# Kernel optimization log

Measured on AMD Instinct MI355X. Metric: run time of the kernel, lower is better.

Reference implementation:

```python
import jax, jax.numpy as jnp
import numpy as np

N = 100000
K = 10  # number of propagation hops


def setup_inputs() -> dict:
    key = jax.random.key(0)
    k1, k2, k3, k4 = jax.random.split(key, 4)
    E, D = 3200000, 128
    feats = jax.random.normal(k1, (N, D), dtype=jnp.float32)
    s = jax.random.normal(k2, (D, 1), dtype=jnp.float32) * 0.1
    src = jax.random.randint(k3, (E,), 0, N, dtype=jnp.int32)
    dst = jax.random.randint(k4, (E,), 0, N, dtype=jnp.int32)
    return {"feats": feats, "s": s, "src": src, "dst": dst}


def reference(feats, s, src, dst):
    # degrees (in-degree = count of dst, out-degree = count of src)
    ones = jnp.ones(src.shape[0], dtype=jnp.float32)
    in_deg = jax.ops.segment_sum(ones, dst, num_segments=N)
    out_deg = jax.ops.segment_sum(ones, src, num_segments=N)
    dst_norm = jnp.clip(in_deg, 1.0, None) ** -0.5  # [N]
    src_norm = jnp.clip(out_deg, 1.0, None) ** -0.5  # [N]
    dst_norm = dst_norm[:, None]
    src_norm = src_norm[:, None]

    results = [feats]
    h = feats
    for _ in range(K):
        h = h * src_norm                                  # [N, D]
        msg = h[src]                                      # gather  [E, D]
        h = jax.ops.segment_sum(msg, dst, num_segments=N)  # scatter [N, D]
        h = h * dst_norm
        results.append(h)

    H = jnp.stack(results, axis=1)                 # [N, K+1, D]
    S = jax.nn.sigmoid(jnp.matmul(H, s))           # [N, K+1, 1]
    S = jnp.transpose(S, (0, 2, 1))                # [N, 1, K+1]
    out = jnp.matmul(S, H).squeeze()               # [N, D]
    return out
```

## Files before the change

### kernel.cpp

```cpp
#include <hip/hip_runtime.h>
#include <hip/hip_fp16.h>

#define NODES 100000
#define DIM 128
#define KSTEPS 10
#define CAP 128

#define RSHIFT 11
#define RANGE 2048
#define NR 49
#define GBCAP 72000
#define VPT 16
#define BT (256 * VPT)

__global__ void bucket_agg(const int* __restrict__ src, const int* __restrict__ dst,
                           unsigned* __restrict__ gdc, unsigned* __restrict__ gsc,
                           unsigned* __restrict__ dpairs, unsigned* __restrict__ spairs, int E) {
    __shared__ unsigned dcnt[NR], scnt[NR], dbase[NR], sbase[NR];
    const int tid = threadIdx.x;
    if (tid < NR) { dcnt[tid] = 0; scnt[tid] = 0; }
    __syncthreads();

    const int base = blockIdx.x * BT;
    int dv[VPT], sv[VPT];
    unsigned rd[VPT], rs[VPT];
    #pragma unroll
    for (int j = 0; j < VPT; ++j) {
        int i = base + tid + j * 256;
        if (i < E) {
            int d_ = dst[i]; int s_ = src[i];
            dv[j] = d_; sv[j] = s_;
            rd[j] = atomicAdd(&dcnt[d_ >> RSHIFT], 1u);
            rs[j] = atomicAdd(&scnt[s_ >> RSHIFT], 1u);
        }
    }
    __syncthreads();
    if (tid < NR) {
        unsigned c = dcnt[tid];
        dbase[tid] = c ? atomicAdd(&gdc[tid], c) : 0u;
    } else if (tid >= 64 && tid < 64 + NR) {
        int b = tid - 64;
        unsigned c = scnt[b];
        sbase[b] = c ? atomicAdd(&gsc[b], c) : 0u;
    }
    __syncthreads();
    #pragma unroll
    for (int j = 0; j < VPT; ++j) {
        int i = base + tid + j * 256;
        if (i < E) {
            int d_ = dv[j]; int s_ = sv[j];
            int b = d_ >> RSHIFT;
            unsigned pos = dbase[b] + rd[j];
            if (pos < GBCAP)
                dpairs[(size_t)b * GBCAP + pos] =
                    ((unsigned)s_ << RSHIFT) | (unsigned)(d_ & (RANGE - 1));
            int bs = s_ >> RSHIFT;
            unsigned ps = sbase[bs] + rs[j];
            if (ps < GBCAP)
                spairs[(size_t)bs * GBCAP + ps] = (unsigned)(s_ & (RANGE - 1));
        }
    }
}

__global__ void degree_scatter(const unsigned* __restrict__ gdc, const unsigned* __restrict__ gsc,
                               const unsigned* __restrict__ dpairs, const unsigned* __restrict__ spairs,
                               int* __restrict__ cur, int* __restrict__ outc,
                               int* __restrict__ csr) {
    __shared__ int ctr[RANGE];
    const int r = blockIdx.x >> 1;
    const int nodebase = r << RSHIFT;
    for (int i = threadIdx.x; i < RANGE; i += blockDim.x) ctr[i] = 0;
    __syncthreads();
    if ((blockIdx.x & 1) == 0) {
        int cnt = (int)gdc[r]; if (cnt > GBCAP) cnt = GBCAP;
        const unsigned* p = dpairs + (size_t)r * GBCAP;
        for (int i = threadIdx.x; i < cnt; i += blockDim.x) {
            unsigned v = p[i];
            int dloc = (int)(v & (RANGE - 1));
            int s_ = (int)(v >> RSHIFT);
            int slot = atomicAdd(&ctr[dloc], 1);
            if (slot < CAP) csr[((size_t)(nodebase + dloc) << 7) + slot] = s_;
        }
        __syncthreads();
        for (int i = threadIdx.x; i < RANGE; i += blockDim.x) {
            int node = nodebase + i;
            if (node < NODES) cur[node] = ctr[i];
        }
    } else {
        int cnt = (int)gsc[r]; if (cnt > GBCAP) cnt = GBCAP;
        const unsigned* p = spairs + (size_t)r * GBCAP;
        for (int i = threadIdx.x; i < cnt; i += blockDim.x)
            atomicAdd(&ctr[p[i]], 1);
        __syncthreads();
        for (int i = threadIdx.x; i < RANGE; i += blockDim.x) {
            int node = nodebase + i;
            if (node < NODES) outc[node] = ctr[i];
        }
    }
}

__global__ void norm_kernel(const int* __restrict__ outc, const int* __restrict__ inc,
                            float* __restrict__ src_norm, float* __restrict__ isrc,
                            float* __restrict__ dst_norm, int n) {
    int i = blockIdx.x * blockDim.x + threadIdx.x;
    if (i < n) {
        float od = fmaxf((float)outc[i], 1.0f);
        float id = fmaxf((float)inc[i], 1.0f);
        float sn = rsqrtf(od);
        src_norm[i] = sn;
        isrc[i] = sqrtf(od);
        dst_norm[i] = rsqrtf(id);
    }
}

__global__ void combine0_main(const float* __restrict__ feats, const float* __restrict__ s,
                              const float* __restrict__ src_norm,
                              __half* __restrict__ p0, float* __restrict__ sg0, int n) {
    int lane = threadIdx.x & 63;
    int wave = (blockIdx.x * blockDim.x + threadIdx.x) >> 6;
    int nwaves = (gridDim.x * blockDim.x) >> 6;
    float2 sv = *(const float2*)(s + lane * 2);
    for (int node = wave; node < n; node += nwaves) {
        float2 hv = *(const float2*)(feats + (size_t)node * DIM + lane * 2);
        float sn = src_norm[node];
        __half2 ph; ph.x = __float2half(sn * hv.x); ph.y = __float2half(sn * hv.y);
        *(__half2*)(p0 + (size_t)node * DIM + lane * 2) = ph;
        float dot = hv.x * sv.x + hv.y * sv.y;
        #pragma unroll
        for (int off = 32; off > 0; off >>= 1) dot += __shfl_xor(dot, off);
        if (lane == 0) sg0[node] = 1.0f / (1.0f + expf(-dot));
    }
}

__global__ void combine0_fb(const float* __restrict__ feats, const float* __restrict__ s,
                            const float* __restrict__ src_norm,
                            __half* __restrict__ p0, float* __restrict__ out, int n) {
    int lane = threadIdx.x & 63;
    int wave = (blockIdx.x * blockDim.x + threadIdx.x) >> 6;
    int nwaves = (gridDim.x * blockDim.x) >> 6;
    float2 sv = *(const float2*)(s + lane * 2);
    for (int node = wave; node < n; node += nwaves) {
        float2 hv = *(const float2*)(feats + (size_t)node * DIM + lane * 2);
        float sn = src_norm[node];
        __half2 ph; ph.x = __float2half(sn * hv.x); ph.y = __float2half(sn * hv.y);
        *(__half2*)(p0 + (size_t)node * DIM + lane * 2) = ph;
        float dot = hv.x * sv.x + hv.y * sv.y;
        #pragma unroll
        for (int off = 32; off > 0; off >>= 1) dot += __shfl_xor(dot, off);
        float sg = 1.0f / (1.0f + expf(-dot));
        float2 ov; ov.x = sg * hv.x; ov.y = sg * hv.y;
        *(float2*)(out + (size_t)node * DIM + lane * 2) = ov;
    }
}

__global__ void gather_main(const __half* __restrict__ pprev,
                            const float* __restrict__ src_norm, const float* __restrict__ dst_norm,
                            const int* __restrict__ cnt, const int* __restrict__ csr,
                            const float* __restrict__ s,
                            __half* __restrict__ pnext, float* __restrict__ sgk, int n) {
    int lane = threadIdx.x & 63;
    int wave = (blockIdx.x * blockDim.x + threadIdx.x) >> 6;
    int nwaves = (gridDim.x * blockDim.x) >> 6;
    float2 sv = *(const float2*)(s + lane * 2);
    for (int node = wave; node < n; node += nwaves) {
        int c = cnt[node]; if (c > CAP) c = CAP;
        const int* row = csr + ((size_t)node << 7);
        float accx = 0.0f, accy = 0.0f;
        int p = 0;
        for (; p + 7 < c; p += 8) {
            int s0 = row[p], s1 = row[p+1], s2 = row[p+2], s3 = row[p+3];
            int s4 = row[p+4], s5 = row[p+5], s6 = row[p+6], s7 = row[p+7];
            float2 f0 = __half22float2(*(const __half2*)(pprev + (size_t)s0 * DIM + lane * 2));
            float2 f1 = __half22float2(*(const __half2*)(pprev + (size_t)s1 * DIM + lane * 2));
            float2 f2 = __half22float2(*(const __half2*)(pprev + (size_t)s2 * DIM + lane * 2));
            float2 f3 = __half22float2(*(const __half2*)(pprev + (size_t)s3 * DIM + lane * 2));
            float2 f4 = __half22float2(*(const __half2*)(pprev + (size_t)s4 * DIM + lane * 2));
            float2 f5 = __half22float2(*(const __half2*)(pprev + (size_t)s5 * DIM + lane * 2));
            float2 f6 = __half22float2(*(const __half2*)(pprev + (size_t)s6 * DIM + lane * 2));
            float2 f7 = __half22float2(*(const __half2*)(pprev + (size_t)s7 * DIM + lane * 2));
            accx += f0.x + f1.x + f2.x + f3.x + f4.x + f5.x + f6.x + f7.x;
            accy += f0.y + f1.y + f2.y + f3.y + f4.y + f5.y + f6.y + f7.y;
        }
        for (; p < c; ++p) {
            int si = row[p];
            float2 fv = __half22float2(*(const __half2*)(pprev + (size_t)si * DIM + lane * 2));
            accx += fv.x; accy += fv.y;
        }
        float dn = dst_norm[node];
        float hx = dn * accx, hy = dn * accy;
        float dot = hx * sv.x + hy * sv.y;
        #pragma unroll
        for (int off = 32; off > 0; off >>= 1) dot += __shfl_xor(dot, off);
        if (lane == 0) sgk[node] = 1.0f / (1.0f + expf(-dot));
        float sn = src_norm[node];
        __half2 pw; pw.x = __float2half(sn * hx); pw.y = __float2half(sn * hy);
        *(__half2*)(pnext + (size_t)node * DIM + lane * 2) = pw;
    }
}

__global__ void gather_fb(const __half* __restrict__ pprev,
                          const float* __restrict__ src_norm, const float* __restrict__ dst_norm,
                          const int* __restrict__ cnt, const int* __restrict__ csr,
                          const float* __restrict__ s,
                          __half* __restrict__ pnext, float* __restrict__ out, int n) {
    int lane = threadIdx.x & 63;
    int wave = (blockIdx.x * blockDim.x + threadIdx.x) >> 6;
    int nwaves = (gridDim.x * blockDim.x) >> 6;
    float2 sv = *(const float2*)(s + lane * 2);
    for (int node = wave; node < n; node += nwaves) {
        int c = cnt[node]; if (c > CAP) c = CAP;
        const int* row = csr + ((size_t)node << 7);
        float accx = 0.0f, accy = 0.0f;
        int p = 0;
        for (; p + 7 < c; p += 8) {
            int s0 = row[p], s1 = row[p+1], s2 = row[p+2], s3 = row[p+3];
            int s4 = row[p+4], s5 = row[p+5], s6 = row[p+6], s7 = row[p+7];
            float2 f0 = __half22float2(*(const __half2*)(pprev + (size_t)s0 * DIM + lane * 2));
            float2 f1 = __half22float2(*(const __half2*)(pprev + (size_t)s1 * DIM + lane * 2));
            float2 f2 = __half22float2(*(const __half2*)(pprev + (size_t)s2 * DIM + lane * 2));
            float2 f3 = __half22float2(*(const __half2*)(pprev + (size_t)s3 * DIM + lane * 2));
            float2 f4 = __half22float2(*(const __half2*)(pprev + (size_t)s4 * DIM + lane * 2));
            float2 f5 = __half22float2(*(const __half2*)(pprev + (size_t)s5 * DIM + lane * 2));
            float2 f6 = __half22float2(*(const __half2*)(pprev + (size_t)s6 * DIM + lane * 2));
            float2 f7 = __half22float2(*(const __half2*)(pprev + (size_t)s7 * DIM + lane * 2));
            accx += f0.x + f1.x + f2.x + f3.x + f4.x + f5.x + f6.x + f7.x;
            accy += f0.y + f1.y + f2.y + f3.y + f4.y + f5.y + f6.y + f7.y;
        }
        for (; p < c; ++p) {
            int si = row[p];
            float2 fv = __half22float2(*(const __half2*)(pprev + (size_t)si * DIM + lane * 2));
            accx += fv.x; accy += fv.y;
        }
        float dn = dst_norm[node];
        float hx = dn * accx, hy = dn * accy;
        float dot = hx * sv.x + hy * sv.y;
        #pragma unroll
        for (int off = 32; off > 0; off >>= 1) dot += __shfl_xor(dot, off);
        float sg = 1.0f / (1.0f + expf(-dot));
        float2 ov = *(float2*)(out + (size_t)node * DIM + lane * 2);
        ov.x += sg * hx; ov.y += sg * hy;
        *(float2*)(out + (size_t)node * DIM + lane * 2) = ov;
        float sn = src_norm[node];
        __half2 pw; pw.x = __float2half(sn * hx); pw.y = __float2half(sn * hy);
        *(__half2*)(pnext + (size_t)node * DIM + lane * 2) = pw;
    }
}

__global__ void out_accum(const __half* __restrict__ pbase, const float* __restrict__ sg,
                          const float* __restrict__ isrc, float* __restrict__ out,
                          int kstart, int count, int m, int first, int n) {
    int lane = threadIdx.x & 63;
    int wave = (blockIdx.x * blockDim.x + threadIdx.x) >> 6;
    int nwaves = (gridDim.x * blockDim.x) >> 6;
    for (int node = wave; node < n; node += nwaves) {
        float iv = isrc[node];
        float ax, ay;
        if (first) { ax = 0.0f; ay = 0.0f; }
        else {
            float2 ov = *(float2*)(out + (size_t)node * DIM + lane * 2);
            ax = ov.x; ay = ov.y;
        }
        for (int j = 0; j < count; ++j) {
            int kk = kstart + j;
            int slot = kk % m;
            float g = sg[(size_t)kk * n + node] * iv;
            float2 fv = __half22float2(
                *(const __half2*)(pbase + ((size_t)slot * n + node) * DIM + lane * 2));
            ax += g * fv.x; ay += g * fv.y;
        }
        *(float2*)(out + (size_t)node * DIM + lane * 2) = make_float2(ax, ay);
    }
}

extern "C" void kernel_launch(void* const* d_in, const int* in_sizes, int n_in,
                              void* d_out, int out_size, void* d_ws, size_t ws_size,
                              hipStream_t stream) {
    const float* feats = (const float*)d_in[0];
    const float* s     = (const float*)d_in[1];
    const int*   src   = (const int*)d_in[2];
    const int*   dst   = (const int*)d_in[3];
    float* out = (float*)d_out;
    const int E = in_sizes[2];

    int*   outc     = (int*)d_ws;
    int*   cur      = outc + NODES;
    float* src_norm = (float*)(cur + NODES);
    float* isrc     = src_norm + NODES;
    float* dst_norm = isrc + NODES;
    float* sg       = dst_norm + NODES;
    int*   csr      = (int*)(sg + (size_t)(KSTEPS + 1) * NODES);
    __half* pbase   = (__half*)(csr + (size_t)NODES * CAP);

    const size_t head_bytes = (size_t)(2 * NODES) * 4 + (size_t)(3 + KSTEPS + 1) * NODES * 4
                            + (size_t)NODES * CAP * 4;
    const size_t pbuf = (size_t)NODES * DIM * sizeof(__half);

    int m = 0;
    if (ws_size > head_bytes) m = (int)((ws_size - head_bytes) / pbuf);
    if (m > KSTEPS + 1) m = KSTEPS + 1;

    unsigned* gdc    = (unsigned*)pbase;
    unsigned* gsc    = gdc + 64;
    unsigned* dpairs = gsc + 64;
    unsigned* spairs = dpairs + (size_t)NR * GBCAP;

    hipMemsetAsync(gdc, 0, 2 * 64 * sizeof(unsigned), stream);
    const int nbatch = (E + BT - 1) / BT;
    bucket_agg<<<nbatch, 256, 0, stream>>>(src, dst, gdc, gsc, dpairs, spairs, E);
    degree_scatter<<<2 * NR, 256, 0, stream>>>(gdc, gsc, dpairs, spairs, cur, outc, csr);
    norm_kernel<<<(NODES + 255) / 256, 256, 0, stream>>>(outc, cur, src_norm, isrc, dst_norm, NODES);

    const int ngrid = (NODES * 64 + 255) / 256;
    if (m >= 2) {
        combine0_main<<<ngrid, 256, 0, stream>>>(feats, s, src_norm, pbase, sg, NODES);
        int flushed = 0;
        int first = 1;
        for (int k = 1; k <= KSTEPS; ++k) {
            if (k - flushed >= m) {
                out_accum<<<ngrid, 256, 0, stream>>>(pbase, sg, isrc, out,
                                                     flushed, k - flushed, m, first, NODES);
                flushed = k; first = 0;
            }
            const __half* pprev = pbase + (size_t)((k - 1) % m) * NODES * DIM;
            __half* pnext = pbase + (size_t)(k % m) * NODES * DIM;
            gather_main<<<ngrid, 256, 0, stream>>>(pprev, src_norm, dst_norm, cur, csr, s,
                                                   pnext, sg + (size_t)k * NODES, NODES);
        }
        out_accum<<<ngrid, 256, 0, stream>>>(pbase, sg, isrc, out,
                                             flushed, KSTEPS + 1 - flushed, m, first, NODES);
    } else {
        __half* pA = pbase;
        __half* pB = pbase + (size_t)NODES * DIM;
        combine0_fb<<<ngrid, 256, 0, stream>>>(feats, s, src_norm, pA, out, NODES);
        const __half* pcur = pA;
        for (int k = 1; k <= KSTEPS; ++k) {
            __half* pnext = (k & 1) ? pB : pA;
            gather_fb<<<ngrid, 256, 0, stream>>>(pcur, src_norm, dst_norm, cur, csr, s,
                                                 pnext, out, NODES);
            pcur = pnext;
        }
    }
}
```

Before: 1.532 ms.

## Gather four neighbor rows per wave with 16-byte loads and padded CSR

Each wave in gather_main is split into four 16-lane groups. Every group fetches a different neighbor row with uint4 loads, so each load instruction covers four edges, and the partial sums are combined afterwards with cross-group shuffles. Neighbor lists are padded to a multiple of 8 with a dummy index pointing at an extra zeroed row per feature slab, which removes the scalar tail loop. CAP drops from 128 to 96 to shrink the CSR footprint. The cost is a few extra memsets and padded loads, plus silent truncation if any node's in-degree exceeds 96.

```diff
diff --git a/kernel.cpp b/kernel.cpp
--- a/kernel.cpp
+++ b/kernel.cpp
@@ -4,7 +4,7 @@
 #define NODES 100000
 #define DIM 128
 #define KSTEPS 10
-#define CAP 128
+#define CAP 96
 
 #define RSHIFT 11
 #define RANGE 2048
@@ -12,6 +12,8 @@
 #define GBCAP 72000
 #define VPT 16
 #define BT (256 * VPT)
+
+#define SLAB ((size_t)(NODES + 1) * DIM)
 
 __global__ void bucket_agg(const int* __restrict__ src, const int* __restrict__ dst,
                            unsigned* __restrict__ gdc, unsigned* __restrict__ gsc,
@@ -79,12 +81,18 @@
             int dloc = (int)(v & (RANGE - 1));
             int s_ = (int)(v >> RSHIFT);
             int slot = atomicAdd(&ctr[dloc], 1);
-            if (slot < CAP) csr[((size_t)(nodebase + dloc) << 7) + slot] = s_;
+            if (slot < CAP) csr[(size_t)(nodebase + dloc) * CAP + slot] = s_;
         }
         __syncthreads();
         for (int i = threadIdx.x; i < RANGE; i += blockDim.x) {
             int node = nodebase + i;
-            if (node < NODES) cur[node] = ctr[i];
+            if (node < NODES) {
+                int c = ctr[i]; if (c > CAP) c = CAP;
+                cur[node] = ctr[i];
+                int cpad = (c + 7) & ~7; if (cpad > CAP) cpad = CAP;
+                for (int q = c; q < cpad; ++q)
+                    csr[(size_t)node * CAP + q] = NODES;
+            }
         }
     } else {
         int cnt = (int)gsc[r]; if (cnt > GBCAP) cnt = GBCAP;
@@ -159,42 +167,84 @@
                             const float* __restrict__ s,
                             __half* __restrict__ pnext, float* __restrict__ sgk, int n) {
     int lane = threadIdx.x & 63;
-    int wave = (blockIdx.x * blockDim.x + threadIdx.x) >> 6;
-    int nwaves = (gridDim.x * blockDim.x) >> 6;
-    float2 sv = *(const float2*)(s + lane * 2);
+    int g = lane >> 4, t = lane & 15;
+    int wave = (blockIdx.x * blockDim.x + threadIdx.x) >> 6;
+    int nwaves = (gridDim.x * blockDim.x) >> 6;
+    float4 sva = *(const float4*)(s + t * 8);
+    float4 svb = *(const float4*)(s + t * 8 + 4);
     for (int node = wave; node < n; node += nwaves) {
         int c = cnt[node]; if (c > CAP) c = CAP;
-        const int* row = csr + ((size_t)node << 7);
-        float accx = 0.0f, accy = 0.0f;
+        int cpad = (c + 7) & ~7;
+        const int* row = csr + (size_t)node * CAP;
+        float a0=0,a1=0,a2=0,a3=0,a4=0,a5=0,a6=0,a7=0;
         int p = 0;
-        for (; p + 7 < c; p += 8) {
-            int s0 = row[p], s1 = row[p+1], s2 = row[p+2], s3 = row[p+3];
-            int s4 = row[p+4], s5 = row[p+5], s6 = row[p+6], s7 = row[p+7];
-            float2 f0 = __half22float2(*(const __half2*)(pprev + (size_t)s0 * DIM + lane * 2));
-            float2 f1 = __half22float2(*(const __half2*)(pprev + (size_t)s1 * DIM + lane * 2));
-            float2 f2 = __half22float2(*(const __half2*)(pprev + (size_t)s2 * DIM + lane * 2));
-            float2 f3 = __half22float2(*(const __half2*)(pprev + (size_t)s3 * DIM + lane * 2));
-            float2 f4 = __half22float2(*(const __half2*)(pprev + (size_t)s4 * DIM + lane * 2));
-            float2 f5 = __half22float2(*(const __half2*)(pprev + (size_t)s5 * DIM + lane * 2));
-            float2 f6 = __half22float2(*(const __half2*)(pprev + (size_t)s6 * DIM + lane * 2));
-            float2 f7 = __half22float2(*(const __half2*)(pprev + (size_t)s7 * DIM + lane * 2));
-            accx += f0.x + f1.x + f2.x + f3.x + f4.x + f5.x + f6.x + f7.x;
-            accy += f0.y + f1.y + f2.y + f3.y + f4.y + f5.y + f6.y + f7.y;
-        }
-        for (; p < c; ++p) {
-            int si = row[p];
-            float2 fv = __half22float2(*(const __half2*)(pprev + (size_t)si * DIM + lane * 2));
-            accx += fv.x; accy += fv.y;
-        }
+        for (; p + 15 < cpad; p += 16) {
+            int e0 = row[p + g];
+            int e1 = row[p + 4 + g];
+            int e2 = row[p + 8 + g];
+            int e3 = row[p + 12 + g];
+            uint4 q0 = *(const uint4*)(pprev + (size_t)e0 * DIM + t * 8);
+            uint4 q1 = *(const uint4*)(pprev + (size_t)e1 * DIM + t * 8);
+            uint4 q2 = *(const uint4*)(pprev + (size_t)e2 * DIM + t * 8);
+            uint4 q3 = *(const uint4*)(pprev + (size_t)e3 * DIM + t * 8);
+            float2 f;
+            f = __half22float2(*(__half2*)&q0.x); a0+=f.x; a1+=f.y;
+            f = __half22float2(*(__half2*)&q0.y); a2+=f.x; a3+=f.y;
+            f = __half22float2(*(__half2*)&q0.z); a4+=f.x; a5+=f.y;
+            f = __half22float2(*(__half2*)&q0.w); a6+=f.x; a7+=f.y;
+            f = __half22float2(*(__half2*)&q1.x); a0+=f.x; a1+=f.y;
+            f = __half22float2(*(__half2*)&q1.y); a2+=f.x; a3+=f.y;
+            f = __half22float2(*(__half2*)&q1.z); a4+=f.x; a5+=f.y;
+            f = __half22float2(*(__half2*)&q1.w); a6+=f.x; a7+=f.y;
+            f = __half22float2(*(__half2*)&q2.x); a0+=f.x; a1+=f.y;
+            f = __half22float2(*(__half2*)&q2.y); a2+=f.x; a3+=f.y;
+            f = __half22float2(*(__half2*)&q2.z); a4+=f.x; a5+=f.y;
+            f = __half22float2(*(__half2*)&q2.w); a6+=f.x; a7+=f.y;
+            f = __half22float2(*(__half2*)&q3.x); a0+=f.x; a1+=f.y;
+            f = __half22float2(*(__half2*)&q3.y); a2+=f.x; a3+=f.y;
+            f = __half22float2(*(__half2*)&q3.z); a4+=f.x; a5+=f.y;
+            f = __half22float2(*(__half2*)&q3.w); a6+=f.x; a7+=f.y;
+        }
+        for (; p < cpad; p += 8) {
+            int e0 = row[p + g];
+            int e1 = row[p + 4 + g];
+            uint4 q0 = *(const uint4*)(pprev + (size_t)e0 * DIM + t * 8);
+            uint4 q1 = *(const uint4*)(pprev + (size_t)e1 * DIM + t * 8);
+            float2 f;
+            f = __half22float2(*(__half2*)&q0.x); a0+=f.x; a1+=f.y;
+            f = __half22float2(*(__half2*)&q0.y); a2+=f.x; a3+=f.y;
+            f = __half22float2(*(__half2*)&q0.z); a4+=f.x; a5+=f.y;
+            f = __half22float2(*(__half2*)&q0.w); a6+=f.x; a7+=f.y;
+            f = __half22float2(*(__half2*)&q1.x); a0+=f.x; a1+=f.y;
+            f = __half22float2(*(__half2*)&q1.y); a2+=f.x; a3+=f.y;
+            f = __half22float2(*(__half2*)&q1.z); a4+=f.x; a5+=f.y;
+            f = __half22float2(*(__half2*)&q1.w); a6+=f.x; a7+=f.y;
+        }
+        a0 += __shfl_xor(a0, 16); a0 += __shfl_xor(a0, 32);
+        a1 += __shfl_xor(a1, 16); a1 += __shfl_xor(a1, 32);
+        a2 += __shfl_xor(a2, 16); a2 += __shfl_xor(a2, 32);
+        a3 += __shfl_xor(a3, 16); a3 += __shfl_xor(a3, 32);
+        a4 += __shfl_xor(a4, 16); a4 += __shfl_xor(a4, 32);
+        a5 += __shfl_xor(a5, 16); a5 += __shfl_xor(a5, 32);
+        a6 += __shfl_xor(a6, 16); a6 += __shfl_xor(a6, 32);
+        a7 += __shfl_xor(a7, 16); a7 += __shfl_xor(a7, 32);
         float dn = dst_norm[node];
-        float hx = dn * accx, hy = dn * accy;
-        float dot = hx * sv.x + hy * sv.y;
-        #pragma unroll
-        for (int off = 32; off > 0; off >>= 1) dot += __shfl_xor(dot, off);
+        float h0=dn*a0, h1=dn*a1, h2=dn*a2, h3=dn*a3;
+        float h4=dn*a4, h5=dn*a5, h6=dn*a6, h7=dn*a7;
+        float dot = h0*sva.x + h1*sva.y + h2*sva.z + h3*sva.w
+                  + h4*svb.x + h5*svb.y + h6*svb.z + h7*svb.w;
+        dot += __shfl_xor(dot, 1); dot += __shfl_xor(dot, 2);
+        dot += __shfl_xor(dot, 4); dot += __shfl_xor(dot, 8);
         if (lane == 0) sgk[node] = 1.0f / (1.0f + expf(-dot));
         float sn = src_norm[node];
-        __half2 pw; pw.x = __float2half(sn * hx); pw.y = __float2half(sn * hy);
-        *(__half2*)(pnext + (size_t)node * DIM + lane * 2) = pw;
+        if (g == 0) {
+            uint4 w;
+            *(__half2*)&w.x = __float22half2_rn(make_float2(sn*h0, sn*h1));
+            *(__half2*)&w.y = __float22half2_rn(make_float2(sn*h2, sn*h3));
+            *(__half2*)&w.z = __float22half2_rn(make_float2(sn*h4, sn*h5));
+            *(__half2*)&w.w = __float22half2_rn(make_float2(sn*h6, sn*h7));
+            *(uint4*)(pnext + (size_t)node * DIM + t * 8) = w;
+        }
     }
 }
 
@@ -209,24 +259,9 @@
     float2 sv = *(const float2*)(s + lane * 2);
     for (int node = wave; node < n; node += nwaves) {
         int c = cnt[node]; if (c > CAP) c = CAP;
-        const int* row = csr + ((size_t)node << 7);
+        const int* row = csr + (size_t)node * CAP;
         float accx = 0.0f, accy = 0.0f;
-        int p = 0;
-        for (; p + 7 < c; p += 8) {
-            int s0 = row[p], s1 = row[p+1], s2 = row[p+2], s3 = row[p+3];
-            int s4 = row[p+4], s5 = row[p+5], s6 = row[p+6], s7 = row[p+7];
-            float2 f0 = __half22float2(*(const __half2*)(pprev + (size_t)s0 * DIM + lane * 2));
-            float2 f1 = __half22float2(*(const __half2*)(pprev + (size_t)s1 * DIM + lane * 2));
-            float2 f2 = __half22float2(*(const __half2*)(pprev + (size_t)s2 * DIM + lane * 2));
-            float2 f3 = __half22float2(*(const __half2*)(pprev + (size_t)s3 * DIM + lane * 2));
-            float2 f4 = __half22float2(*(const __half2*)(pprev + (size_t)s4 * DIM + lane * 2));
-            float2 f5 = __half22float2(*(const __half2*)(pprev + (size_t)s5 * DIM + lane * 2));
-            float2 f6 = __half22float2(*(const __half2*)(pprev + (size_t)s6 * DIM + lane * 2));
-            float2 f7 = __half22float2(*(const __half2*)(pprev + (size_t)s7 * DIM + lane * 2));
-            accx += f0.x + f1.x + f2.x + f3.x + f4.x + f5.x + f6.x + f7.x;
-            accy += f0.y + f1.y + f2.y + f3.y + f4.y + f5.y + f6.y + f7.y;
-        }
-        for (; p < c; ++p) {
+        for (int p = 0; p < c; ++p) {
             int si = row[p];
             float2 fv = __half22float2(*(const __half2*)(pprev + (size_t)si * DIM + lane * 2));
             accx += fv.x; accy += fv.y;
@@ -265,7 +300,7 @@
             int slot = kk % m;
             float g = sg[(size_t)kk * n + node] * iv;
             float2 fv = __half22float2(
-                *(const __half2*)(pbase + ((size_t)slot * n + node) * DIM + lane * 2));
+                *(const __half2*)(pbase + (size_t)slot * SLAB + (size_t)node * DIM + lane * 2));
             ax += g * fv.x; ay += g * fv.y;
         }
         *(float2*)(out + (size_t)node * DIM + lane * 2) = make_float2(ax, ay);
@@ -293,7 +328,7 @@
 
     const size_t head_bytes = (size_t)(2 * NODES) * 4 + (size_t)(3 + KSTEPS + 1) * NODES * 4
                             + (size_t)NODES * CAP * 4;
-    const size_t pbuf = (size_t)NODES * DIM * sizeof(__half);
+    const size_t pbuf = SLAB * sizeof(__half);
 
     int m = 0;
     if (ws_size > head_bytes) m = (int)((ws_size - head_bytes) / pbuf);
@@ -312,6 +347,10 @@
 
     const int ngrid = (NODES * 64 + 255) / 256;
     if (m >= 2) {
+        for (int slot = 0; slot < m; ++slot)
+            hipMemsetAsync(pbase + (size_t)slot * SLAB + (size_t)NODES * DIM, 0,
+                           DIM * sizeof(__half), stream);
+
         combine0_main<<<ngrid, 256, 0, stream>>>(feats, s, src_norm, pbase, sg, NODES);
         int flushed = 0;
         int first = 1;
@@ -321,8 +360,8 @@
                                                      flushed, k - flushed, m, first, NODES);
                 flushed = k; first = 0;
             }
-            const __half* pprev = pbase + (size_t)((k - 1) % m) * NODES * DIM;
-            __half* pnext = pbase + (size_t)(k % m) * NODES * DIM;
+            const __half* pprev = pbase + (size_t)((k - 1) % m) * SLAB;
+            __half* pnext = pbase + (size_t)(k % m) * SLAB;
             gather_main<<<ngrid, 256, 0, stream>>>(pprev, src_norm, dst_norm, cur, csr, s,
                                                    pnext, sg + (size_t)k * NODES, NODES);
         }
@@ -330,7 +369,7 @@
                                              flushed, KSTEPS + 1 - flushed, m, first, NODES);
     } else {
         __half* pA = pbase;
-        __half* pB = pbase + (size_t)NODES * DIM;
+        __half* pB = pbase + SLAB;
         combine0_fb<<<ngrid, 256, 0, stream>>>(feats, s, src_norm, pA, out, NODES);
         const __half* pcur = pA;
         for (int k = 1; k <= KSTEPS; ++k) {
```

After: 1.414 ms. 7.7% less time.
